# Kernel optimization log

Hardware: AMD Instinct MI355X
Metric: run time of the kernel (lower is better)

The kernel has to match this reference:

```python
import jax, jax.numpy as jnp
import numpy as np

B, D, C, T = 2, 1024, 256, 32
H = 8
F = C // H
E = 1024  # time_embed_dim
GROUPS = 32
SCALE = F ** -0.5


def group_norm(x, scale, bias):
    # x: [B, D, C, T]; GroupNorm(32, C) over (channels-in-group, T)
    b, d, c, t = x.shape
    xg = x.reshape(b, d, GROUPS, c // GROUPS, t)
    m = xg.mean(axis=(3, 4), keepdims=True)
    v = xg.var(axis=(3, 4), keepdims=True)
    xn = ((xg - m) * jax.lax.rsqrt(v + 1e-5)).reshape(b, d, c, t)
    return xn * scale[None, None, :, None] + bias[None, None, :, None]


def rpe_R(temb, pairwise, dw, db, tw, tb, ow, ob):
    # pairwise: [B, T, T] int -> R: [B, T, T, H, F]
    pd = pairwise.astype(jnp.float32)
    dist_embs = jnp.stack([
        jnp.log1p(jnp.maximum(pd, 0.0)),
        jnp.log1p(jnp.maximum(-pd, 0.0)),
        (pairwise == 0).astype(jnp.float32),
    ], axis=-1)  # [B, T, T, 3]
    emb = (temb @ tw.T + tb)[:, :, None, :] + (dist_embs @ dw.T + db)  # [B,T,T,C]
    r = jax.nn.silu(emb) @ ow.T + ob
    return r.reshape(r.shape[0], r.shape[1], r.shape[2], H, F)


def setup_inputs() -> dict:
    key = jax.random.key(0)
    ks = jax.random.split(key, 20)
    s = 0.02
    inp = {
        "x": jax.random.normal(ks[0], (B, D, C, T), jnp.float32),
        "temb": jax.random.normal(ks[1], (B, T, E), jnp.float32),
        "norm_scale": jnp.ones((C,), jnp.float32),
        "norm_bias": jnp.zeros((C,), jnp.float32),
        "qkv_w": jax.random.normal(ks[2], (3 * C, C), jnp.float32) * s,
        "qkv_b": jnp.zeros((3 * C,), jnp.float32),
        "proj_w": jax.random.normal(ks[3], (C, C), jnp.float32) * s,
        "proj_b": jnp.zeros((C,), jnp.float32),
        # stacked RPE params for (q, k, v) nets
        "rpe_dist_w": jax.random.normal(ks[4], (3, C, 3), jnp.float32) * s,
        "rpe_dist_b": jnp.zeros((3, C), jnp.float32),
        "rpe_time_w": jax.random.normal(ks[5], (3, C, E), jnp.float32) * s,
        "rpe_time_b": jnp.zeros((3, C), jnp.float32),
        "rpe_out_w": jax.random.normal(ks[6], (3, C, C), jnp.float32) * s,
        "rpe_out_b": jax.random.normal(ks[7], (3, C), jnp.float32) * s,
        "frame_indices": jnp.sort(jax.random.randint(ks[8], (B, T), 0, 100), axis=-1),
    }
    return inp


def reference(x, temb, norm_scale, norm_bias, qkv_w, qkv_b, proj_w, proj_b,
              rpe_dist_w, rpe_dist_b, rpe_time_w, rpe_time_b, rpe_out_w, rpe_out_b,
              frame_indices):
    xn = group_norm(x, norm_scale, norm_bias)          # [B,D,C,T]
    xt = jnp.einsum('BDCT->BDTC', xn)                  # [B,D,T,C]
    qkv = (xt @ qkv_w.T + qkv_b).reshape(B, D, T, 3, H, F)
    qkv = jnp.einsum('BDTtHF->tBDHTF', qkv)
    q, k, v = qkv[0] * SCALE, qkv[1], qkv[2]           # [B,D,H,T,F]

    attn = jnp.einsum('bdhtf,bdhsf->bdhts', q, k)

    pairwise = frame_indices[:, :, None] - frame_indices[:, None, :]  # [B,T,T]
    R_q = rpe_R(temb, pairwise, rpe_dist_w[0], rpe_dist_b[0], rpe_time_w[0], rpe_time_b[0], rpe_out_w[0], rpe_out_b[0])
    R_k = rpe_R(temb, pairwise, rpe_dist_w[1], rpe_dist_b[1], rpe_time_w[1], rpe_time_b[1], rpe_out_w[1], rpe_out_b[1])
    R_v = rpe_R(temb, pairwise, rpe_dist_w[2], rpe_dist_b[2], rpe_time_w[2], rpe_time_b[2], rpe_out_w[2], rpe_out_b[2])

    attn = attn + jnp.einsum('bdhtf,btshf->bdhts', q, R_k)
    # rpe_q: forward_qk on (k*scale) then transpose last two dims
    attn = attn + jnp.einsum('bdhtf,btshf->bdhts', k * SCALE, R_q).swapaxes(-1, -2)

    attn = jax.nn.softmax(attn.astype(jnp.float32), axis=-1).astype(attn.dtype)

    out = jnp.einsum('bdhts,bdhsf->bdhtf', attn, v)
    out = out + jnp.einsum('bdhts,btshf->bdhtf', attn, R_v)

    out = jnp.einsum('BDHTF->BDTHF', out).reshape(B, D, T, C)
    out = out @ proj_w.T + proj_b
    y = xt + out                                       # residual on post-norm x (as in source)
    return jnp.einsum('BDTC->BDCT', y)
```

## Files before the change

kernel.cpp:

```cpp
#include <hip/hip_runtime.h>

#define BB 2
#define DD 1024
#define CC 256
#define TT 32
#define HH 8
#define FF 32
#define EE 1024
#define SCALE 0.17677669529663687f

typedef unsigned short u16;
typedef unsigned int u32;
typedef __attribute__((ext_vector_type(8))) short s8v;
typedef __attribute__((ext_vector_type(4))) float f32x4;

static __device__ __forceinline__ float u2f(u16 u) {
  return __uint_as_float(((u32)u) << 16);
}
static __device__ __forceinline__ u16 f2u(float f) {
  u32 x = __float_as_uint(f);
  x += 0x7fffu + ((x >> 16) & 1u);
  return (u16)(x >> 16);
}
static __device__ __forceinline__ float dot2bf(u32 a, u32 b, float c) {
  float d;
  asm("v_dot2_f32_bf16 %0, %1, %2, %3" : "=v"(d) : "v"(a), "v"(b), "v"(c));
  return d;
}
#define D2(acc, a, b) acc = dot2bf(a, b, acc)

static __device__ __forceinline__ float logits_r(
    const u16* kr,
    uint4 r0, uint4 r1, uint4 r2, uint4 r3,
    uint4 r4, uint4 r5, uint4 r6, uint4 r7,
    uint4 q0, uint4 q1, uint4 q2, uint4 q3) {
  uint4 k0 = *(const uint4*)(kr + 0);
  uint4 k1 = *(const uint4*)(kr + 8);
  uint4 k2 = *(const uint4*)(kr + 16);
  uint4 k3 = *(const uint4*)(kr + 24);
  float xq = 0.f, xr = 0.f, xk = 0.f;
  D2(xq, q0.x, k0.x); D2(xq, q0.y, k0.y); D2(xq, q0.z, k0.z); D2(xq, q0.w, k0.w);
  D2(xq, q1.x, k1.x); D2(xq, q1.y, k1.y); D2(xq, q1.z, k1.z); D2(xq, q1.w, k1.w);
  D2(xq, q2.x, k2.x); D2(xq, q2.y, k2.y); D2(xq, q2.z, k2.z); D2(xq, q2.w, k2.w);
  D2(xq, q3.x, k3.x); D2(xq, q3.y, k3.y); D2(xq, q3.z, k3.z); D2(xq, q3.w, k3.w);
  D2(xr, q0.x, r0.x); D2(xr, q0.y, r0.y); D2(xr, q0.z, r0.z); D2(xr, q0.w, r0.w);
  D2(xr, q1.x, r1.x); D2(xr, q1.y, r1.y); D2(xr, q1.z, r1.z); D2(xr, q1.w, r1.w);
  D2(xr, q2.x, r2.x); D2(xr, q2.y, r2.y); D2(xr, q2.z, r2.z); D2(xr, q2.w, r2.w);
  D2(xr, q3.x, r3.x); D2(xr, q3.y, r3.y); D2(xr, q3.z, r3.z); D2(xr, q3.w, r3.w);
  D2(xk, k0.x, r4.x); D2(xk, k0.y, r4.y); D2(xk, k0.z, r4.z); D2(xk, k0.w, r4.w);
  D2(xk, k1.x, r5.x); D2(xk, k1.y, r5.y); D2(xk, k1.z, r5.z); D2(xk, k1.w, r5.w);
  D2(xk, k2.x, r6.x); D2(xk, k2.y, r6.y); D2(xk, k2.z, r6.z); D2(xk, k2.w, r6.w);
  D2(xk, k3.x, r7.x); D2(xk, k3.y, r7.y); D2(xk, k3.z, r7.z); D2(xk, k3.w, r7.w);
  return xq + xr + xk;
}

static __device__ __forceinline__ float pv_r(
    uint4 p0, uint4 p1, uint4 p2, uint4 p3,
    const u16* vr, uint4 r0, uint4 r1, uint4 r2, uint4 r3) {
  uint4 v0 = *(const uint4*)(vr + 0),  v1 = *(const uint4*)(vr + 8);
  uint4 v2 = *(const uint4*)(vr + 16), v3 = *(const uint4*)(vr + 24);
  float o = 0.f;
  D2(o, p0.x, v0.x); D2(o, p0.y, v0.y); D2(o, p0.z, v0.z); D2(o, p0.w, v0.w);
  D2(o, p1.x, v1.x); D2(o, p1.y, v1.y); D2(o, p1.z, v1.z); D2(o, p1.w, v1.w);
  D2(o, p2.x, v2.x); D2(o, p2.y, v2.y); D2(o, p2.z, v2.z); D2(o, p2.w, v2.w);
  D2(o, p3.x, v3.x); D2(o, p3.y, v3.y); D2(o, p3.z, v3.z); D2(o, p3.w, v3.w);
  D2(o, p0.x, r0.x); D2(o, p0.y, r0.y); D2(o, p0.z, r0.z); D2(o, p0.w, r0.w);
  D2(o, p1.x, r1.x); D2(o, p1.y, r1.y); D2(o, p1.z, r1.z); D2(o, p1.w, r1.w);
  D2(o, p2.x, r2.x); D2(o, p2.y, r2.y); D2(o, p2.z, r2.z); D2(o, p2.w, r2.w);
  D2(o, p3.x, r3.x); D2(o, p3.y, r3.y); D2(o, p3.z, r3.z); D2(o, p3.w, r3.w);
  return o;
}

#define LOADROW8(P, v0, v1, v2, v3, v4, v5, v6, v7)                      \
  v0 = *(const uint4*)((P) + 0);  v1 = *(const uint4*)((P) + 8);         \
  v2 = *(const uint4*)((P) + 16); v3 = *(const uint4*)((P) + 24);        \
  v4 = *(const uint4*)((P) + 32); v5 = *(const uint4*)((P) + 40);        \
  v6 = *(const uint4*)((P) + 48); v7 = *(const uint4*)((P) + 56);
#define LOADROW4(P, v0, v1, v2, v3)                                      \
  v0 = *(const uint4*)((P) + 0);  v1 = *(const uint4*)((P) + 8);         \
  v2 = *(const uint4*)((P) + 16); v3 = *(const uint4*)((P) + 24);

__global__ __launch_bounds__(256, 4) void k_f0(
    const float* __restrict__ x, const float* __restrict__ nsc,
    const float* __restrict__ nbi, u16* __restrict__ pun,
    const float* __restrict__ qw, const float* __restrict__ pw,
    const float* __restrict__ ow, const float* __restrict__ tw,
    const float* __restrict__ temb, const float* __restrict__ tb,
    const float* __restrict__ dw, const float* __restrict__ db,
    const int* __restrict__ fidx,
    u16* __restrict__ wpk2, u16* __restrict__ ppk, u16* __restrict__ opk,
    u16* __restrict__ E) {
  const int bid = blockIdx.x;
  const int tid = threadIdx.x;
  __shared__ u16 xt[TT][264];
  __shared__ float st[EE];
  __shared__ float base_s[CC];
  __shared__ int sfi[TT];

  if (bid < 2048) {
    int xcd = bid & 7, jj = bid >> 3;
    int b = xcd >> 2;
    int d = (xcd & 3) * 256 + jj;
    const size_t xbase = ((size_t)(b * DD + d)) * 8192;
    u16* xnp = pun + xbase * 2 + 8192;
    {
      const int c0 = tid >> 3, tq = tid & 7;
      for (int c = c0; c < CC; c += 32) {
        float4 v = *(const float4*)(x + xbase + (size_t)c * TT + tq * 4);
        xt[tq * 4 + 0][c] = f2u(v.x);
        xt[tq * 4 + 1][c] = f2u(v.y);
        xt[tq * 4 + 2][c] = f2u(v.z);
        xt[tq * 4 + 3][c] = f2u(v.w);
      }
    }
    __syncthreads();
    {
      const int c = tid;
      float s = 0.f, s2 = 0.f;
      for (int t = 0; t < TT; ++t) { float v = u2f(xt[t][c]); s += v; s2 += v * v; }
      s += __shfl_xor(s, 1); s2 += __shfl_xor(s2, 1);
      s += __shfl_xor(s, 2); s2 += __shfl_xor(s2, 2);
      s += __shfl_xor(s, 4); s2 += __shfl_xor(s2, 4);
      const float mean = s * (1.f / 256.f);
      const float var = s2 * (1.f / 256.f) - mean * mean;
      const float rs = rsqrtf(var + 1e-5f);
      const float scv = nsc[c] * rs;
      const float biv = nbi[c] - mean * scv;
      for (int t = 0; t < TT; ++t) xt[t][c] = f2u(u2f(xt[t][c]) * scv + biv);
    }
    __syncthreads();
#pragma unroll
    for (int it = 0; it < 4; ++it) {
      int u = it * 256 + tid;
      int t = u >> 5, c = (u & 31) * 8;
      *(uint4*)(xnp + (size_t)u * 8) = *(const uint4*)&xt[t][c];
    }
  } else if (bid < 2272) {
    int id = (bid - 2048) * 256 + tid;
    if (id < 24576) {
      int lane = id & 63, ks = (id >> 6) & 7, tile = id >> 9;
      int hh = tile / 6, r = tile % 6, sec = r >> 1, nt = r & 1;
      int nrow = sec * 256 + hh * 32 + nt * 16 + (lane & 15);
      int k = ks * 32 + (lane >> 4) * 8;
      const float* src = qw + (size_t)nrow * 256 + k;
      u16* dst = wpk2 + (size_t)id * 8;
#pragma unroll
      for (int e = 0; e < 8; ++e) dst[e] = f2u(src[e]);
    } else if (id < 32768) {
      int j = id - 24576;
      int lane = j & 63, ks = (j >> 6) & 7, nt = j >> 9;
      int row = nt * 16 + (lane & 15);
      int k = ks * 32 + (lane >> 4) * 8;
      const float* src = pw + (size_t)row * 256 + k;
      u16* dst = ppk + (size_t)j * 8;
#pragma unroll
      for (int e = 0; e < 8; ++e) dst[e] = f2u(src[e]);
    } else {
      int j = id - 32768;
      int lane = j & 63, ks = (j >> 6) & 7, g = j >> 9;
      int n = g >> 4, ntg = g & 15;
      int row = ntg * 16 + (lane & 15);
      int k = ks * 32 + (lane >> 4) * 8;
      const float* src = ow + ((size_t)n * 256 + row) * 256 + k;
      u16* dst = opk + (size_t)j * 8;
#pragma unroll
      for (int e = 0; e < 8; ++e) dst[e] = f2u(src[e]);
    }
  } else {
    int bid3 = bid - 2272;
    int t = bid3 & 31, b = (bid3 >> 5) & 1, n = bid3 >> 6;
    for (int e = tid; e < EE; e += 256)
      st[e] = temb[((size_t)b * TT + t) * EE + e];
    if (tid < TT) sfi[tid] = fidx[b * TT + tid];
    __syncthreads();
    const int g = tid & 7, cl = tid >> 3;
#pragma unroll
    for (int pass = 0; pass < 8; ++pass) {
      const int c = pass * 32 + cl;
      const float* wr = tw + ((size_t)n * 256 + c) * 1024 + g * 4;
      float acc = 0.f;
      for (int step = 0; step < 32; ++step) {
        float4 wv = *(const float4*)(wr + step * 32);
        float4 sv = *(const float4*)(st + g * 4 + step * 32);
        acc += sv.x * wv.x + sv.y * wv.y + sv.z * wv.z + sv.w * wv.w;
      }
      acc += __shfl_xor(acc, 1);
      acc += __shfl_xor(acc, 2);
      acc += __shfl_xor(acc, 4);
      if (g == 0) base_s[c] = acc;
    }
    __syncthreads();
    const int c = tid;
    float base = base_s[c] + tb[n * 256 + c] + db[n * 256 + c];
    float dw0 = dw[(n * 256 + c) * 3 + 0];
    float dw1 = dw[(n * 256 + c) * 3 + 1];
    float dw2 = dw[(n * 256 + c) * 3 + 2];
    int ft = sfi[t];
    u16* erow = E + ((size_t)n * 2048 + b * 1024 + t * 32) * 256 + c;
    for (int s = 0; s < TT; ++s) {
      int pd = ft - sfi[s];
      float d0 = log1pf((float)(pd > 0 ? pd : 0));
      float d1 = log1pf((float)(pd < 0 ? -pd : 0));
      float d2 = (pd == 0) ? 1.f : 0.f;
      float e = base + d0 * dw0 + d1 * dw1 + d2 * dw2;
      float se = e / (1.f + expf(-e));
      erow[(size_t)s * 256] = f2u(se);
    }
  }
}

__global__ __launch_bounds__(256) void k_rgemm(
    const u16* __restrict__ E, const u16* __restrict__ opk,
    const float* __restrict__ ob,
    u16* __restrict__ RKQ, u16* __restrict__ Rv) {
  int bid = blockIdx.x;
  int n = bid >> 6, rem = bid & 63;
  int mblk = rem >> 1, nblk = rem & 1;
  int tid = threadIdx.x;
  int w = tid >> 6, lane = tid & 63;
  int l15 = lane & 15, l4 = lane >> 4;
  size_t rowbase = (size_t)n * 2048 + mblk * 64;

  f32x4 acc[2][4];
#pragma unroll
  for (int i = 0; i < 2; ++i) {
    int ntg = nblk * 8 + w * 2 + i;
    float ov = ob[n * 256 + ntg * 16 + l15];
#pragma unroll
    for (int mt = 0; mt < 4; ++mt) acc[i][mt] = (f32x4){ov, ov, ov, ov};
  }
  for (int ks = 0; ks < 8; ++ks) {
    s8v a[4];
#pragma unroll
    for (int mt = 0; mt < 4; ++mt)
      a[mt] = *(const s8v*)(E + (rowbase + mt * 16 + l15) * 256 + ks * 32 + l4 * 8);
#pragma unroll
    for (int i = 0; i < 2; ++i) {
      int ntg = nblk * 8 + w * 2 + i;
      s8v bf = *(const s8v*)(opk + (((size_t)(n * 16 + ntg) * 8 + ks) * 64 + lane) * 8);
#pragma unroll
      for (int mt = 0; mt < 4; ++mt)
        acc[i][mt] = __builtin_amdgcn_mfma_f32_16x16x32_bf16(a[mt], bf, acc[i][mt], 0, 0, 0);
    }
  }
#pragma unroll
  for (int i = 0; i < 2; ++i) {
    int cc = (nblk * 8 + w * 2 + i) * 16 + l15;
    int hh = cc >> 5, f = cc & 31;
#pragma unroll
    for (int mt = 0; mt < 4; ++mt)
#pragma unroll
      for (int r = 0; r < 4; ++r) {
        int rloc = mblk * 64 + mt * 16 + l4 * 4 + r;
        int bb2 = rloc >> 10, tt = (rloc >> 5) & 31, ss = rloc & 31;
        size_t bh = (size_t)(bb2 * 8 + hh);
        float v = acc[i][mt][r];
        if (n == 0)      RKQ[(bh * 1024 + ss * 32 + tt) * 64 + 32 + f] = f2u(v * SCALE);
        else if (n == 1) RKQ[(bh * 1024 + tt * 32 + ss) * 64 + f] = f2u(v);
        else             Rv[((bh * 32 + tt) * 32 + f) * 32 + ss] = f2u(v);
      }
  }
}

__global__ __launch_bounds__(256, 3) void k_attn(
    u16* __restrict__ pun, const u16* __restrict__ wpk2,
    const float* __restrict__ qkb,
    const u16* __restrict__ RKQ, const u16* __restrict__ Rv) {
  int bid = blockIdx.x;
  int xcd = bid & 7, i5 = bid >> 3;
  int b = xcd >> 2;
  int h = i5 & 7;
  int dg = (xcd & 3) * 64 + (i5 >> 3);
  int d0 = dg * 4;
  const int tid = threadIdx.x;
  __shared__ u16 xsbuf[32 * 260];
  __shared__ u16 qs[4][32][40];
  __shared__ u16 ks_[4][32][40];
  __shared__ u16 vT[4][32][40];
#define XS_(r, c)   xsbuf[(r) * 260 + (c)]
#define ATSP(d, t)  (xsbuf + ((d) * 32 + (t)) * 40)

  const int w = tid >> 6, lane = tid & 63;
  const int l15 = lane & 15, l4 = lane >> 4;
  const int t = tid >> 3, j = tid & 7;
  const size_t bh = (size_t)(b * 8 + h);
  const u16* rp0 = RKQ + (bh * 1024 + (size_t)t * 32 + j) * 64;
  const u16* rv0 = Rv + ((bh * 32 + (size_t)t) * 32 + j) * 32;

  u16* slot0 = pun + ((size_t)(b * DD + d0)) * 16384;

  const u16* xp0 = slot0 + 8192;
  uint4 xr0 = *(const uint4*)(xp0 + (size_t)tid * 8);
  uint4 xr1 = *(const uint4*)(xp0 + (size_t)(256 + tid) * 8);
  uint4 xr2 = *(const uint4*)(xp0 + (size_t)(512 + tid) * 8);
  uint4 xr3 = *(const uint4*)(xp0 + (size_t)(768 + tid) * 8);

  uint4 A0, A1, A2, A3, A4, A5, A6, A7;

#pragma unroll
  for (int d = 0; d < 4; ++d) {
    *(uint4*)&XS_((tid >> 5), (tid & 31) * 8) = xr0;
    *(uint4*)&XS_(8 + (tid >> 5), (tid & 31) * 8) = xr1;
    *(uint4*)&XS_(16 + (tid >> 5), (tid & 31) * 8) = xr2;
    *(uint4*)&XS_(24 + (tid >> 5), (tid & 31) * 8) = xr3;
    __syncthreads();
    if (d < 3) {
      const u16* nx = slot0 + (size_t)(d + 1) * 16384 + 8192;
      xr0 = *(const uint4*)(nx + (size_t)tid * 8);
      xr1 = *(const uint4*)(nx + (size_t)(256 + tid) * 8);
      xr2 = *(const uint4*)(nx + (size_t)(512 + tid) * 8);
      xr3 = *(const uint4*)(nx + (size_t)(768 + tid) * 8);
    }
#pragma unroll
    for (int i = 0; i < 3; ++i) {
      const int u = w * 3 + i;
      const int sec = u >> 2;
      const int nt = (u >> 1) & 1;
      const int mh = u & 1;
      f32x4 acc = {0.f, 0.f, 0.f, 0.f};
      const u16* wb = wpk2 + ((size_t)((h * 6 + sec * 2 + nt) * 8) * 64 + lane) * 8;
#pragma unroll
      for (int ks = 0; ks < 8; ++ks) {
        s8v a = *(const s8v*)&XS_(mh * 16 + l15, ks * 32 + l4 * 8);
        s8v bf = *(const s8v*)(wb + (size_t)ks * 512);
        acc = __builtin_amdgcn_mfma_f32_16x16x32_bf16(a, bf, acc, 0, 0, 0);
      }
      const int f = nt * 16 + l15;
      const float bias = qkb[sec * 256 + h * 32 + f];
      if (sec == 2) {
        ushort4 pk;
        pk.x = f2u(acc[0] + bias);
        pk.y = f2u(acc[1] + bias);
        pk.z = f2u(acc[2] + bias);
        pk.w = f2u(acc[3] + bias);
        *(ushort4*)&vT[d][f][mh * 16 + l4 * 4] = pk;
      } else {
#pragma unroll
        for (int r = 0; r < 4; ++r) {
          const int tt = mh * 16 + l4 * 4 + r;
          const float val = acc[r] + bias;
          if (sec == 0) qs[d][tt][f] = f2u(val * SCALE);
          else          ks_[d][tt][f] = f2u(val);
        }
      }
    }
    if (d == 3) {
      LOADROW8(rp0, A0, A1, A2, A3, A4, A5, A6, A7)
    }
    __syncthreads();
  }

  uint4 q[4][4];
#pragma unroll
  for (int d = 0; d < 4; ++d) {
    q[d][0] = *(const uint4*)&qs[d][t][0];
    q[d][1] = *(const uint4*)&qs[d][t][8];
    q[d][2] = *(const uint4*)&qs[d][t][16];
    q[d][3] = *(const uint4*)&qs[d][t][24];
  }
  float a[4][4];
  uint4 B0, B1, B2, B3, B4, B5, B6, B7;
  LOADROW8(rp0 + 8 * 64, B0, B1, B2, B3, B4, B5, B6, B7)
#pragma unroll
  for (int d = 0; d < 4; ++d)
    a[d][0] = logits_r(&ks_[d][j][0], A0, A1, A2, A3, A4, A5, A6, A7,
                       q[d][0], q[d][1], q[d][2], q[d][3]);
  LOADROW8(rp0 + 16 * 64, A0, A1, A2, A3, A4, A5, A6, A7)
#pragma unroll
  for (int d = 0; d < 4; ++d)
    a[d][1] = logits_r(&ks_[d][j + 8][0], B0, B1, B2, B3, B4, B5, B6, B7,
                       q[d][0], q[d][1], q[d][2], q[d][3]);
  LOADROW8(rp0 + 24 * 64, B0, B1, B2, B3, B4, B5, B6, B7)
#pragma unroll
  for (int d = 0; d < 4; ++d)
    a[d][2] = logits_r(&ks_[d][j + 16][0], A0, A1, A2, A3, A4, A5, A6, A7,
                       q[d][0], q[d][1], q[d][2], q[d][3]);
#pragma unroll
  for (int d = 0; d < 4; ++d)
    a[d][3] = logits_r(&ks_[d][j + 24][0], B0, B1, B2, B3, B4, B5, B6, B7,
                       q[d][0], q[d][1], q[d][2], q[d][3]);

#pragma unroll
  for (int d = 0; d < 4; ++d) {
    float mx = fmaxf(fmaxf(a[d][0], a[d][1]), fmaxf(a[d][2], a[d][3]));
    mx = fmaxf(mx, __shfl_xor(mx, 1));
    mx = fmaxf(mx, __shfl_xor(mx, 2));
    mx = fmaxf(mx, __shfl_xor(mx, 4));
    float e0 = __expf(a[d][0] - mx), e1 = __expf(a[d][1] - mx);
    float e2 = __expf(a[d][2] - mx), e3 = __expf(a[d][3] - mx);
    float sum = e0 + e1 + e2 + e3;
    sum += __shfl_xor(sum, 1);
    sum += __shfl_xor(sum, 2);
    sum += __shfl_xor(sum, 4);
    const float inv = 1.f / sum;
    u16* ap = ATSP(d, t);
    ap[j]      = f2u(e0 * inv);
    ap[j + 8]  = f2u(e1 * inv);
    ap[j + 16] = f2u(e2 * inv);
    ap[j + 24] = f2u(e3 * inv);
  }

  uint4 p[4][4];
#pragma unroll
  for (int d = 0; d < 4; ++d) {
    const u16* ap = ATSP(d, t);
    p[d][0] = *(const uint4*)(ap + 0);
    p[d][1] = *(const uint4*)(ap + 8);
    p[d][2] = *(const uint4*)(ap + 16);
    p[d][3] = *(const uint4*)(ap + 24);
  }
  float o[4][4];
  uint4 VA0, VA1, VA2, VA3, VB0, VB1, VB2, VB3;
  LOADROW4(rv0,          VA0, VA1, VA2, VA3)
  LOADROW4(rv0 + 8 * 32, VB0, VB1, VB2, VB3)
#pragma unroll
  for (int d = 0; d < 4; ++d)
    o[d][0] = pv_r(p[d][0], p[d][1], p[d][2], p[d][3], &vT[d][j][0],
                   VA0, VA1, VA2, VA3);
  LOADROW4(rv0 + 16 * 32, VA0, VA1, VA2, VA3)
#pragma unroll
  for (int d = 0; d < 4; ++d)
    o[d][1] = pv_r(p[d][0], p[d][1], p[d][2], p[d][3], &vT[d][j + 8][0],
                   VB0, VB1, VB2, VB3);
  LOADROW4(rv0 + 24 * 32, VB0, VB1, VB2, VB3)
#pragma unroll
  for (int d = 0; d < 4; ++d)
    o[d][2] = pv_r(p[d][0], p[d][1], p[d][2], p[d][3], &vT[d][j + 16][0],
                   VA0, VA1, VA2, VA3);
#pragma unroll
  for (int d = 0; d < 4; ++d)
    o[d][3] = pv_r(p[d][0], p[d][1], p[d][2], p[d][3], &vT[d][j + 24][0],
                   VB0, VB1, VB2, VB3);

#pragma unroll
  for (int d = 0; d < 4; ++d) {
    u16* op = slot0 + (size_t)d * 16384 + (size_t)t * 256 + h * 32 + j;
    op[0]  = f2u(o[d][0]);
    op[8]  = f2u(o[d][1]);
    op[16] = f2u(o[d][2]);
    op[24] = f2u(o[d][3]);
  }
#undef XS_
#undef ATSP
}

__global__ __launch_bounds__(256, 4) void k_proj(
    u16* __restrict__ pun, const u16* __restrict__ ppk,
    const float* __restrict__ pb, float* __restrict__ out) {
  int bid = blockIdx.x;
  int xcd = bid & 7, jj = bid >> 3;
  int b = xcd >> 2;
  int d = (xcd & 3) * 256 + jj;
  const int tid = threadIdx.x;
  __shared__ u16 obuf[32][264];
  __shared__ u16 xs[32][264];
  const size_t nbase = ((size_t)(b * DD + d)) * 8192;
  u16* slot = pun + nbase * 2;
#pragma unroll
  for (int it = 0; it < 4; ++it) {
    int u = it * 256 + tid;
    int t = u >> 5, c = (u & 31) * 8;
    *(uint4*)&obuf[t][c] = *(const uint4*)(slot + (size_t)u * 8);
    *(uint4*)&xs[t][c]   = *(const uint4*)(slot + 8192 + (size_t)u * 8);
  }
  __syncthreads();

  const int w = tid >> 6, lane = tid & 63;
  const int l15 = lane & 15, l4 = lane >> 4;
  f32x4 pacc[4][2];
#pragma unroll
  for (int i = 0; i < 4; ++i) {
    pacc[i][0] = (f32x4){0.f, 0.f, 0.f, 0.f};
    pacc[i][1] = (f32x4){0.f, 0.f, 0.f, 0.f};
  }
  for (int ks = 0; ks < 8; ++ks) {
    s8v a0 = *(const s8v*)&obuf[l15][ks * 32 + l4 * 8];
    s8v a1 = *(const s8v*)&obuf[16 + l15][ks * 32 + l4 * 8];
#pragma unroll
    for (int i = 0; i < 4; ++i) {
      s8v bf = *(const s8v*)(ppk + ((size_t)((w * 4 + i) * 8 + ks) * 64 + lane) * 8);
      pacc[i][0] = __builtin_amdgcn_mfma_f32_16x16x32_bf16(a0, bf, pacc[i][0], 0, 0, 0);
      pacc[i][1] = __builtin_amdgcn_mfma_f32_16x16x32_bf16(a1, bf, pacc[i][1], 0, 0, 0);
    }
  }
#pragma unroll
  for (int i = 0; i < 4; ++i) {
    const int co = (w * 4 + i) * 16 + l15;
    const float pbv = pb[co];
#pragma unroll
    for (int mt = 0; mt < 2; ++mt) {
      const int t0 = mt * 16 + l4 * 4;
      float4 sv;
      sv.x = pacc[i][mt][0] + u2f(xs[t0 + 0][co]) + pbv;
      sv.y = pacc[i][mt][1] + u2f(xs[t0 + 1][co]) + pbv;
      sv.z = pacc[i][mt][2] + u2f(xs[t0 + 2][co]) + pbv;
      sv.w = pacc[i][mt][3] + u2f(xs[t0 + 3][co]) + pbv;
      *(float4*)(out + nbase + (size_t)co * TT + t0) = sv;
    }
  }
}

extern "C" void kernel_launch(void* const* d_in, const int* in_sizes, int n_in,
                              void* d_out, int out_size, void* d_ws, size_t ws_size,
                              hipStream_t stream) {
  const float* x      = (const float*)d_in[0];
  const float* temb   = (const float*)d_in[1];
  const float* nsc    = (const float*)d_in[2];
  const float* nbi    = (const float*)d_in[3];
  const float* qkv_w  = (const float*)d_in[4];
  const float* qkv_b  = (const float*)d_in[5];
  const float* proj_w = (const float*)d_in[6];
  const float* proj_b = (const float*)d_in[7];
  const float* dw     = (const float*)d_in[8];
  const float* db     = (const float*)d_in[9];
  const float* tw     = (const float*)d_in[10];
  const float* tb     = (const float*)d_in[11];
  const float* ow     = (const float*)d_in[12];
  const float* ob     = (const float*)d_in[13];
  const int*   fidx   = (const int*)d_in[14];
  float* out = (float*)d_out;
  u16* pun = (u16*)d_out;

  u16* wpk2 = (u16*)d_ws;
  u16* ppk  = wpk2 + 196608;
  u16* opk  = ppk + 65536;
  u16* E    = opk + 196608;
  u16* RKQ  = E + 1572864;
  u16* Rv   = RKQ + 1048576;

  k_f0<<<2464, 256, 0, stream>>>(x, nsc, nbi, pun, qkv_w, proj_w, ow, tw,
                                 temb, tb, dw, db, fidx, wpk2, ppk, opk, E);
  k_rgemm<<<192, 256, 0, stream>>>(E, opk, ob, RKQ, Rv);
  k_attn<<<4096, 256, 0, stream>>>(pun, wpk2, qkv_b, RKQ, Rv);
  k_proj<<<2048, 256, 0, stream>>>(pun, ppk, proj_b, out);
}
```

Baseline: 218.3 us.

## Move QK^T and PV products onto MFMA, keep RPE terms on dot2

The plain q·k logits and P·V products are now computed per head with 16x16x32 bf16 MFMA instructions, one wave per d slice. Results are staged through shared memory (the attention buffer and the reused ks_ buffer) and added to the scalar RPE dot2 terms. This removes half of the v_dot2 work in the logits and PV stages. In exchange it adds two extra __syncthreads, LDS round trips, and bf16 rounding of the intermediate QK and PV partial sums.

```diff
diff --git a/kernel.cpp b/kernel.cpp
--- a/kernel.cpp
+++ b/kernel.cpp
@@ -29,7 +29,7 @@
 }
 #define D2(acc, a, b) acc = dot2bf(a, b, acc)
 
-static __device__ __forceinline__ float logits_r(
+static __device__ __forceinline__ float logits_rx(
     const u16* kr,
     uint4 r0, uint4 r1, uint4 r2, uint4 r3,
     uint4 r4, uint4 r5, uint4 r6, uint4 r7,
@@ -38,11 +38,7 @@
   uint4 k1 = *(const uint4*)(kr + 8);
   uint4 k2 = *(const uint4*)(kr + 16);
   uint4 k3 = *(const uint4*)(kr + 24);
-  float xq = 0.f, xr = 0.f, xk = 0.f;
-  D2(xq, q0.x, k0.x); D2(xq, q0.y, k0.y); D2(xq, q0.z, k0.z); D2(xq, q0.w, k0.w);
-  D2(xq, q1.x, k1.x); D2(xq, q1.y, k1.y); D2(xq, q1.z, k1.z); D2(xq, q1.w, k1.w);
-  D2(xq, q2.x, k2.x); D2(xq, q2.y, k2.y); D2(xq, q2.z, k2.z); D2(xq, q2.w, k2.w);
-  D2(xq, q3.x, k3.x); D2(xq, q3.y, k3.y); D2(xq, q3.z, k3.z); D2(xq, q3.w, k3.w);
+  float xr = 0.f, xk = 0.f;
   D2(xr, q0.x, r0.x); D2(xr, q0.y, r0.y); D2(xr, q0.z, r0.z); D2(xr, q0.w, r0.w);
   D2(xr, q1.x, r1.x); D2(xr, q1.y, r1.y); D2(xr, q1.z, r1.z); D2(xr, q1.w, r1.w);
   D2(xr, q2.x, r2.x); D2(xr, q2.y, r2.y); D2(xr, q2.z, r2.z); D2(xr, q2.w, r2.w);
@@ -51,19 +47,13 @@
   D2(xk, k1.x, r5.x); D2(xk, k1.y, r5.y); D2(xk, k1.z, r5.z); D2(xk, k1.w, r5.w);
   D2(xk, k2.x, r6.x); D2(xk, k2.y, r6.y); D2(xk, k2.z, r6.z); D2(xk, k2.w, r6.w);
   D2(xk, k3.x, r7.x); D2(xk, k3.y, r7.y); D2(xk, k3.z, r7.z); D2(xk, k3.w, r7.w);
-  return xq + xr + xk;
-}
-
-static __device__ __forceinline__ float pv_r(
+  return xr + xk;
+}
+
+static __device__ __forceinline__ float pv_rv(
     uint4 p0, uint4 p1, uint4 p2, uint4 p3,
-    const u16* vr, uint4 r0, uint4 r1, uint4 r2, uint4 r3) {
-  uint4 v0 = *(const uint4*)(vr + 0),  v1 = *(const uint4*)(vr + 8);
-  uint4 v2 = *(const uint4*)(vr + 16), v3 = *(const uint4*)(vr + 24);
+    uint4 r0, uint4 r1, uint4 r2, uint4 r3) {
   float o = 0.f;
-  D2(o, p0.x, v0.x); D2(o, p0.y, v0.y); D2(o, p0.z, v0.z); D2(o, p0.w, v0.w);
-  D2(o, p1.x, v1.x); D2(o, p1.y, v1.y); D2(o, p1.z, v1.z); D2(o, p1.w, v1.w);
-  D2(o, p2.x, v2.x); D2(o, p2.y, v2.y); D2(o, p2.z, v2.z); D2(o, p2.w, v2.w);
-  D2(o, p3.x, v3.x); D2(o, p3.y, v3.y); D2(o, p3.z, v3.z); D2(o, p3.w, v3.w);
   D2(o, p0.x, r0.x); D2(o, p0.y, r0.y); D2(o, p0.z, r0.z); D2(o, p0.w, r0.w);
   D2(o, p1.x, r1.x); D2(o, p1.y, r1.y); D2(o, p1.z, r1.z); D2(o, p1.w, r1.w);
   D2(o, p2.x, r2.x); D2(o, p2.y, r2.y); D2(o, p2.z, r2.z); D2(o, p2.w, r2.w);
@@ -350,6 +340,28 @@
     __syncthreads();
   }
 
+  {
+    const int d = w;
+    s8v aq0 = *(const s8v*)&qs[d][l15][l4 * 8];
+    s8v aq1 = *(const s8v*)&qs[d][16 + l15][l4 * 8];
+    s8v bk0 = *(const s8v*)&ks_[d][l15][l4 * 8];
+    s8v bk1 = *(const s8v*)&ks_[d][16 + l15][l4 * 8];
+    const f32x4 z = {0.f, 0.f, 0.f, 0.f};
+    f32x4 c00 = __builtin_amdgcn_mfma_f32_16x16x32_bf16(aq0, bk0, z, 0, 0, 0);
+    f32x4 c01 = __builtin_amdgcn_mfma_f32_16x16x32_bf16(aq0, bk1, z, 0, 0, 0);
+    f32x4 c10 = __builtin_amdgcn_mfma_f32_16x16x32_bf16(aq1, bk0, z, 0, 0, 0);
+    f32x4 c11 = __builtin_amdgcn_mfma_f32_16x16x32_bf16(aq1, bk1, z, 0, 0, 0);
+#pragma unroll
+    for (int r = 0; r < 4; ++r) {
+      const int t0r = l4 * 4 + r, t1r = 16 + l4 * 4 + r;
+      ATSP(d, t0r)[l15]      = f2u(c00[r]);
+      ATSP(d, t0r)[16 + l15] = f2u(c01[r]);
+      ATSP(d, t1r)[l15]      = f2u(c10[r]);
+      ATSP(d, t1r)[16 + l15] = f2u(c11[r]);
+    }
+  }
+  __syncthreads();
+
   uint4 q[4][4];
 #pragma unroll
   for (int d = 0; d < 4; ++d) {
@@ -363,22 +375,26 @@
   LOADROW8(rp0 + 8 * 64, B0, B1, B2, B3, B4, B5, B6, B7)
 #pragma unroll
   for (int d = 0; d < 4; ++d)
-    a[d][0] = logits_r(&ks_[d][j][0], A0, A1, A2, A3, A4, A5, A6, A7,
-                       q[d][0], q[d][1], q[d][2], q[d][3]);
+    a[d][0] = u2f(ATSP(d, t)[j]) +
+              logits_rx(&ks_[d][j][0], A0, A1, A2, A3, A4, A5, A6, A7,
+                        q[d][0], q[d][1], q[d][2], q[d][3]);
   LOADROW8(rp0 + 16 * 64, A0, A1, A2, A3, A4, A5, A6, A7)
 #pragma unroll
   for (int d = 0; d < 4; ++d)
-    a[d][1] = logits_r(&ks_[d][j + 8][0], B0, B1, B2, B3, B4, B5, B6, B7,
-                       q[d][0], q[d][1], q[d][2], q[d][3]);
+    a[d][1] = u2f(ATSP(d, t)[j + 8]) +
+              logits_rx(&ks_[d][j + 8][0], B0, B1, B2, B3, B4, B5, B6, B7,
+                        q[d][0], q[d][1], q[d][2], q[d][3]);
   LOADROW8(rp0 + 24 * 64, B0, B1, B2, B3, B4, B5, B6, B7)
 #pragma unroll
   for (int d = 0; d < 4; ++d)
-    a[d][2] = logits_r(&ks_[d][j + 16][0], A0, A1, A2, A3, A4, A5, A6, A7,
-                       q[d][0], q[d][1], q[d][2], q[d][3]);
-#pragma unroll
-  for (int d = 0; d < 4; ++d)
-    a[d][3] = logits_r(&ks_[d][j + 24][0], B0, B1, B2, B3, B4, B5, B6, B7,
-                       q[d][0], q[d][1], q[d][2], q[d][3]);
+    a[d][2] = u2f(ATSP(d, t)[j + 16]) +
+              logits_rx(&ks_[d][j + 16][0], A0, A1, A2, A3, A4, A5, A6, A7,
+                        q[d][0], q[d][1], q[d][2], q[d][3]);
+#pragma unroll
+  for (int d = 0; d < 4; ++d)
+    a[d][3] = u2f(ATSP(d, t)[j + 24]) +
+              logits_rx(&ks_[d][j + 24][0], B0, B1, B2, B3, B4, B5, B6, B7,
+                        q[d][0], q[d][1], q[d][2], q[d][3]);
 
 #pragma unroll
   for (int d = 0; d < 4; ++d) {
@@ -399,6 +415,29 @@
     ap[j + 16] = f2u(e2 * inv);
     ap[j + 24] = f2u(e3 * inv);
   }
+  __syncthreads();
+
+  {
+    const int d = w;
+    s8v pa0 = *(const s8v*)(ATSP(d, l15) + l4 * 8);
+    s8v pa1 = *(const s8v*)(ATSP(d, 16 + l15) + l4 * 8);
+    s8v vb0 = *(const s8v*)&vT[d][l15][l4 * 8];
+    s8v vb1 = *(const s8v*)&vT[d][16 + l15][l4 * 8];
+    const f32x4 z = {0.f, 0.f, 0.f, 0.f};
+    f32x4 c00 = __builtin_amdgcn_mfma_f32_16x16x32_bf16(pa0, vb0, z, 0, 0, 0);
+    f32x4 c01 = __builtin_amdgcn_mfma_f32_16x16x32_bf16(pa0, vb1, z, 0, 0, 0);
+    f32x4 c10 = __builtin_amdgcn_mfma_f32_16x16x32_bf16(pa1, vb0, z, 0, 0, 0);
+    f32x4 c11 = __builtin_amdgcn_mfma_f32_16x16x32_bf16(pa1, vb1, z, 0, 0, 0);
+#pragma unroll
+    for (int r = 0; r < 4; ++r) {
+      const int t0r = l4 * 4 + r, t1r = 16 + l4 * 4 + r;
+      ks_[d][t0r][l15]      = f2u(c00[r]);
+      ks_[d][t0r][16 + l15] = f2u(c01[r]);
+      ks_[d][t1r][l15]      = f2u(c10[r]);
+      ks_[d][t1r][16 + l15] = f2u(c11[r]);
+    }
+  }
+  __syncthreads();
 
   uint4 p[4][4];
 #pragma unroll
@@ -415,22 +454,22 @@
   LOADROW4(rv0 + 8 * 32, VB0, VB1, VB2, VB3)
 #pragma unroll
   for (int d = 0; d < 4; ++d)
-    o[d][0] = pv_r(p[d][0], p[d][1], p[d][2], p[d][3], &vT[d][j][0],
-                   VA0, VA1, VA2, VA3);
+    o[d][0] = u2f(ks_[d][t][j]) +
+              pv_rv(p[d][0], p[d][1], p[d][2], p[d][3], VA0, VA1, VA2, VA3);
   LOADROW4(rv0 + 16 * 32, VA0, VA1, VA2, VA3)
 #pragma unroll
   for (int d = 0; d < 4; ++d)
-    o[d][1] = pv_r(p[d][0], p[d][1], p[d][2], p[d][3], &vT[d][j + 8][0],
-                   VB0, VB1, VB2, VB3);
+    o[d][1] = u2f(ks_[d][t][j + 8]) +
+              pv_rv(p[d][0], p[d][1], p[d][2], p[d][3], VB0, VB1, VB2, VB3);
   LOADROW4(rv0 + 24 * 32, VB0, VB1, VB2, VB3)
 #pragma unroll
   for (int d = 0; d < 4; ++d)
-    o[d][2] = pv_r(p[d][0], p[d][1], p[d][2], p[d][3], &vT[d][j + 16][0],
-                   VA0, VA1, VA2, VA3);
-#pragma unroll
-  for (int d = 0; d < 4; ++d)
-    o[d][3] = pv_r(p[d][0], p[d][1], p[d][2], p[d][3], &vT[d][j + 24][0],
-                   VB0, VB1, VB2, VB3);
+    o[d][2] = u2f(ks_[d][t][j + 16]) +
+              pv_rv(p[d][0], p[d][1], p[d][2], p[d][3], VA0, VA1, VA2, VA3);
+#pragma unroll
+  for (int d = 0; d < 4; ++d)
+    o[d][3] = u2f(ks_[d][t][j + 24]) +
+              pv_rv(p[d][0], p[d][1], p[d][2], p[d][3], VB0, VB1, VB2, VB3);
 
 #pragma unroll
   for (int d = 0; d < 4; ++d) {
```

Result: slower. 239.2 us (+9.6%).
